# Performance work log

Hardware: AMD Instinct MI355X
Metric: run time of the kernel (lower is better)

The kernel has to match this reference:

```python
import jax, jax.numpy as jnp
import numpy as np

# Geometry: 256x256 image, 16x16 superpixel grid (cell=16), K=256, C=20 features, B=4.
B, H, W, C, KG = 4, 256, 256, 20, 16
K = KG * KG
CELL = H // KG
BIG_DIST = 1e4  # additive distance for non-neighbor superpixels


def setup_inputs() -> dict:
    key = jax.random.key(0)
    kf, = jax.random.split(key, 1)
    # initial hard pixel->superpixel grid assignment (get_spixel_init)
    gy = jnp.arange(H) // CELL
    gx = jnp.arange(W) // CELL
    spixel_init = (gy[:, None] * KG + gx[None, :]).reshape(-1).astype(jnp.int32)  # [N]
    # 9-neighborhood validity mask (compute_neighbor_spix_idx)
    ky = jnp.arange(K) // KG
    kx = jnp.arange(K) % KG
    pgy = spixel_init // KG
    pgx = spixel_init % KG
    valid = ((jnp.abs(pgy[:, None] - ky[None, :]) <= 1)
             & (jnp.abs(pgx[:, None] - kx[None, :]) <= 1)).astype(jnp.float32)  # [N, K]
    adjust = (1.0 - valid) * BIG_DIST  # [N, K]
    features = jax.random.normal(kf, (B, H * W, C), dtype=jnp.float32)  # CNN output, flattened
    return {
        "features": features,
        "valid_spixel": valid,
        "adjust_dist": adjust,
        "spixel_init": spixel_init,
        "iter_EM": 10,
    }


def _e_step(mean, features, valid_spixel, adjust_dist):
    # squared distances via ||f||^2 - 2 f.m + ||m||^2 (bmm form)
    feat_sq = jnp.sum(features * features, axis=-1)        # [B, N]
    mean_sq = jnp.sum(mean * mean, axis=-1)                # [B, K]
    dot = jnp.einsum('bnc,bkc->bnk', features, mean)       # [B, N, K]
    dist_sq = feat_sq[:, :, None] - 2.0 * dot + mean_sq[:, None, :]
    dist_sq = dist_sq * valid_spixel[None] + adjust_dist[None]
    # std = 1/sqrt(2) => 2*std^2 = 1, so softmax argument is -dist_sq
    return jax.nn.softmax(-dist_sq, axis=2)                # [B, N, K]


def _m_step(features, posteriors):
    # L1-normalize posteriors over the pixel axis (dim=1), then weighted mean
    col = jnp.maximum(jnp.sum(posteriors, axis=1, keepdims=True), 1e-12)
    post_norm = posteriors / col
    return jnp.einsum('bnk,bnc->bkc', post_norm, features)  # [B, K, C]


def reference(features, valid_spixel, adjust_dist, spixel_init, iter_EM):
    # compute_init_spixel_feat: mean of features within each initial superpixel (detached in torch)
    n = features.shape[1]
    sums = jax.vmap(lambda f: jax.ops.segment_sum(f, spixel_init, num_segments=K))(features)  # [B, K, C]
    counts = jax.ops.segment_sum(jnp.ones((n,), features.dtype), spixel_init, num_segments=K)  # [K]
    mean = jax.lax.stop_gradient(sums / jnp.maximum(counts, 1.0)[None, :, None])
    for _ in range(int(iter_EM) - 1):
        posteriors = _e_step(mean, features, valid_spixel, adjust_dist)
        mean = _m_step(features, posteriors)
    return _e_step(mean, features, valid_spixel, adjust_dist)
```

## Files before the change

kernel.cpp:

```cpp
#include <hip/hip_runtime.h>


#define NBATCH 4
#define WIMG   256
#define NC     20
#define NCS    21
#define NKG    16
#define NK     256
#define NPIX   65536
#define CELLSZ 16
#define LDST   260
#define NBLK   (NBATCH * NK)
#define CPAD   64
#define NCTRL  (NBATCH * NK)

typedef float nfloat4 __attribute__((ext_vector_type(4)));

__device__ __forceinline__ float dot4f(const float4 a, const float4 b) {
    return fmaf(a.x, b.x, fmaf(a.y, b.y, fmaf(a.z, b.z, a.w * b.w)));
}

__device__ __forceinline__ float sys_load(const float* p) {
    return __hip_atomic_load(p, __ATOMIC_RELAXED, __HIP_MEMORY_SCOPE_SYSTEM);
}
__device__ __forceinline__ void sys_store(float* p, float v) {
    __hip_atomic_store(p, v, __ATOMIC_RELAXED, __HIP_MEMORY_SCOPE_SYSTEM);
}
__device__ __forceinline__ unsigned sys_loadu(const unsigned* p) {
    return __hip_atomic_load(p, __ATOMIC_RELAXED, __HIP_MEMORY_SCOPE_SYSTEM);
}

__device__ __forceinline__ void wait_slots(const unsigned* ctr, unsigned gen,
                                           int b, int cy, int cx, int t) {
    if (t < 9) {
        int ky = cy + t / 3 - 1, kx = cx + (t % 3) - 1;
        if (ky >= 0 && ky < NKG && kx >= 0 && kx < NKG) {
            int ry = 1 + (ky > 0) + (ky < NKG - 1);
            int rx = 1 + (kx > 0) + (kx < NKG - 1);
            unsigned tgt = gen * (unsigned)(ry * rx);
            const unsigned* p = ctr + (size_t)(b * NK + ky * NKG + kx) * CPAD;
            unsigned long long t0 = __builtin_amdgcn_s_memrealtime();
            while (sys_loadu(p) < tgt) {
                __builtin_amdgcn_s_sleep(2);
                if (__builtin_amdgcn_s_memrealtime() - t0 > 10000000ull) break;
            }
        }
    }
    __syncthreads();
}

__device__ __forceinline__ void signal_slots(unsigned* ctr, int b, int cy, int cx, int t) {
    if (t < 9) {
        int ky = cy + t / 3 - 1, kx = cx + (t % 3) - 1;
        if (ky >= 0 && ky < NKG && kx >= 0 && kx < NKG)
            __hip_atomic_fetch_add(ctr + (size_t)(b * NK + ky * NKG + kx) * CPAD, 1u,
                                   __ATOMIC_RELAXED, __HIP_MEMORY_SCOPE_SYSTEM);
    }
}

__device__ __forceinline__ void load_feat(const float* __restrict__ feat, int b, int n, float f[NC]) {
    const float4* fp = (const float4*)(feat + ((size_t)b * NPIX + n) * NC);
    #pragma unroll
    for (int i = 0; i < 5; ++i) {
        float4 v = fp[i];
        f[4 * i + 0] = v.x; f[4 * i + 1] = v.y; f[4 * i + 2] = v.z; f[4 * i + 3] = v.w;
    }
}

__device__ __forceinline__ void stage_neigh(const float* __restrict__ Sprev, int b, int cy, int cx,
                                            int t, float (*sM)[24], float (*rqs)[2]) {
    if (t < 189) {
        int j = t / 21, c = t - 21 * j;
        int ky = cy + j / 3 - 1, kx = cx + (j % 3) - 1;
        float v = 0.0f;
        if (ky >= 0 && ky < NKG && kx >= 0 && kx < NKG)
            v = sys_load(&Sprev[((size_t)(b * NK + ky * NKG + kx)) * NCS + c]);
        sM[j][c] = v;
    }
    __syncthreads();
    if (t < 9) {
        int ky = cy + t / 3 - 1, kx = cx + (t % 3) - 1;
        bool ok = (ky >= 0 && ky < NKG && kx >= 0 && kx < NKG);
        float ssq = 0.f;
        #pragma unroll
        for (int cq = 0; cq < 5; ++cq) {
            float4 sv = *((const float4*)&sM[t][4 * cq]);
            ssq += dot4f(sv, sv);
        }
        float r = 1.0f / fmaxf(sM[t][NC], 1e-12f);
        rqs[t][0] = ok ? 2.0f * r : 0.0f;
        rqs[t][1] = ok ? -(r * r) * ssq : -1e30f;
    }
    __syncthreads();
}

__device__ __forceinline__ void e_step_lds(const float f[NC], const float (*sM)[24],
                                           const float (*rqs)[2], float p[9]) {
    float a[9];
    float amax = -1e30f;
    #pragma unroll
    for (int j = 0; j < 9; ++j) {
        float dots = 0.f;
        #pragma unroll
        for (int cq = 0; cq < 5; ++cq) {
            float4 sv = *((const float4*)&sM[j][4 * cq]);
            dots = fmaf(f[4 * cq + 0], sv.x,
                   fmaf(f[4 * cq + 1], sv.y,
                   fmaf(f[4 * cq + 2], sv.z,
                   fmaf(f[4 * cq + 3], sv.w, dots))));
        }
        float2 rv = *((const float2*)rqs[j]);
        a[j] = fmaf(rv.x, dots, rv.y);
        amax = fmaxf(amax, a[j]);
    }
    float esum = 0.f;
    #pragma unroll
    for (int j = 0; j < 9; ++j) {
        float e = (a[j] > -1e29f) ? __expf(a[j] - amax) : 0.0f;
        p[j] = e;
        esum += e;
    }
    float inv = 1.0f / esum;
    #pragma unroll
    for (int j = 0; j < 9; ++j) p[j] *= inv;
}

__global__ void k_zero_ctr(unsigned* ctr) {
    int i = blockIdx.x * 256 + threadIdx.x;
    if (i < NCTRL) ctr[(size_t)i * CPAD] = 0u;
}

__global__ __launch_bounds__(256, 4) void k_fused(const float* __restrict__ feat,
                                                  float* __restrict__ b0,
                                                  float* __restrict__ b1,
                                                  float* __restrict__ b2,
                                                  unsigned* __restrict__ ctr,
                                                  float* __restrict__ out) {
    __shared__ float fT[NCS * LDST];
    __shared__ float pT[9 * LDST];
    __shared__ float part[21 * 8 * 9];
    __shared__ float sM[9][24];
    __shared__ float rqs[9][2];

    int blk = blockIdx.x;
    int b = blk >> 8, k0 = blk & 255;
    int cy = k0 >> 4, cx = k0 & 15;
    int t = threadIdx.x;
    int ly = t >> 4, lx = t & 15;
    int n = (cy * CELLSZ + ly) * WIMG + cx * CELLSZ + lx;

    float f[NC];
    load_feat(feat, b, n, f);
    #pragma unroll
    for (int c = 0; c < NC; ++c) fT[c * LDST + t] = f[c];
    fT[NC * LDST + t] = 1.0f;
    __syncthreads();

    if (t < NCS) {
        float s;
        if (t == NC) {
            s = 256.0f;
        } else {
            s = 0.f;
            const float4* row = (const float4*)&fT[t * LDST];
            #pragma unroll 4
            for (int i = 0; i < 64; ++i) { float4 v = row[i]; s += v.x + v.y + v.z + v.w; }
        }
        size_t off = ((size_t)(b * NK + k0)) * NCS + t;
        sys_store(&b0[off], s);
        sys_store(&b1[off], 0.0f);
    }
    __syncthreads();
    signal_slots(ctr, b, cy, cx, t);
    unsigned gen = 1;

    float* Sprev = b0; float* Snext = b1; float* Szero = b2;

    for (int it = 0; it < 9; ++it) {
        wait_slots(ctr, gen, b, cy, cx, t);
        stage_neigh(Sprev, b, cy, cx, t, sM, rqs);

        float p[9];
        e_step_lds(f, sM, rqs, p);
        #pragma unroll
        for (int j = 0; j < 9; ++j) pT[j * LDST + t] = p[j];
        __syncthreads();

        if (t < 168) {
            int tile = t >> 3, kid = t & 7;
            int j0 = (tile / 7) * 3, c0 = (tile % 7) * 3;
            float acc[3][3] = {};
            #pragma unroll
            for (int ch = 0; ch < 8; ++ch) {
                int nb = kid * 32 + (((ch + kid) & 7) << 2);
                float4 pv[3], fv[3];
                #pragma unroll
                for (int jj = 0; jj < 3; ++jj) pv[jj] = *(const float4*)&pT[(j0 + jj) * LDST + nb];
                #pragma unroll
                for (int cc = 0; cc < 3; ++cc) fv[cc] = *(const float4*)&fT[(c0 + cc) * LDST + nb];
                #pragma unroll
                for (int jj = 0; jj < 3; ++jj)
                    #pragma unroll
                    for (int cc = 0; cc < 3; ++cc)
                        acc[jj][cc] += dot4f(pv[jj], fv[cc]);
            }
            #pragma unroll
            for (int jj = 0; jj < 3; ++jj)
                #pragma unroll
                for (int cc = 0; cc < 3; ++cc)
                    part[tile * 72 + kid * 9 + jj * 3 + cc] = acc[jj][cc];
        }
        __syncthreads();
        if (t < 189) {
            int j = t / 21, c = t - 21 * j;
            int tile = (j / 3) * 7 + (c / 3);
            int elem = (j % 3) * 3 + (c % 3);
            float s = 0.f;
            #pragma unroll
            for (int kid = 0; kid < 8; ++kid) s += part[tile * 72 + kid * 9 + elem];
            int ky = cy + (j / 3) - 1, kx = cx + (j % 3) - 1;
            if (ky >= 0 && ky < NKG && kx >= 0 && kx < NKG)
                atomicAdd(&Snext[((size_t)(b * NK + ky * NKG + kx)) * NCS + c], s);
        }
        if (t < NCS) sys_store(&Szero[((size_t)(b * NK + k0)) * NCS + t], 0.0f);
        __syncthreads();
        signal_slots(ctr, b, cy, cx, t);
        ++gen;
        float* tmp = Sprev; Sprev = Snext; Snext = Szero; Szero = tmp;
    }

    wait_slots(ctr, gen, b, cy, cx, t);
    stage_neigh(Sprev, b, cy, cx, t, sM, rqs);
    {
        float p[9];
        e_step_lds(f, sM, rqs, p);
        #pragma unroll
        for (int j = 0; j < 9; ++j) pT[j * LDST + t] = p[j];
    }
    __syncthreads();

    int wv = t >> 6, ln = t & 63;
    int j4[4];
    #pragma unroll
    for (int q = 0; q < 4; ++q) {
        int k = 4 * ln + q;
        int ky = k >> 4, kx = k & 15;
        int dy = ky - cy, dx = kx - cx;
        j4[q] = (dy >= -1 && dy <= 1 && dx >= -1 && dx <= 1) ? (dy + 1) * 3 + (dx + 1) : -1;
    }
    for (int i = 0; i < 64; ++i) {
        int pix = wv * 64 + i;
        int py = pix >> 4, px = pix & 15;
        int np = (cy * CELLSZ + py) * WIMG + cx * CELLSZ + px;
        nfloat4 o;
        o.x = (j4[0] >= 0) ? pT[j4[0] * LDST + pix] : 0.0f;
        o.y = (j4[1] >= 0) ? pT[j4[1] * LDST + pix] : 0.0f;
        o.z = (j4[2] >= 0) ? pT[j4[2] * LDST + pix] : 0.0f;
        o.w = (j4[3] >= 0) ? pT[j4[3] * LDST + pix] : 0.0f;
        size_t rowoff = ((size_t)(b * NPIX + np)) * (size_t)NK;
        __builtin_nontemporal_store(o, (nfloat4*)(out + rowoff + 4 * ln));
    }
}


__device__ __forceinline__ void e_step_global(const float* f, int b, int cy, int cx,
                                              const float* __restrict__ Sprev, float p[9]) {
    float a[9];
    float amax = -1e30f;
    #pragma unroll
    for (int dy = -1; dy <= 1; ++dy) {
        #pragma unroll
        for (int dx = -1; dx <= 1; ++dx) {
            int j = (dy + 1) * 3 + (dx + 1);
            int ky = cy + dy, kx = cx + dx;
            if (ky >= 0 && ky < NKG && kx >= 0 && kx < NKG) {
                const float* sp = Sprev + ((size_t)(b * NK + ky * NKG + kx)) * NCS;
                float dots = 0.f, ssq = 0.f;
                #pragma unroll
                for (int c = 0; c < NC; ++c) {
                    float sv = sp[c];
                    dots = fmaf(f[c], sv, dots);
                    ssq  = fmaf(sv, sv, ssq);
                }
                float col = fmaxf(sp[NC], 1e-12f);
                float r = 1.0f / col;
                a[j] = 2.0f * r * dots - (r * r) * ssq;
                amax = fmaxf(amax, a[j]);
            } else {
                a[j] = -1e30f;
            }
        }
    }
    float esum = 0.f;
    #pragma unroll
    for (int j = 0; j < 9; ++j) {
        float e = (a[j] > -1e29f) ? __expf(a[j] - amax) : 0.0f;
        p[j] = e;
        esum += e;
    }
    float inv = 1.0f / esum;
    #pragma unroll
    for (int j = 0; j < 9; ++j) p[j] *= inv;
}

__global__ __launch_bounds__(256, 4) void k_init(const float* __restrict__ feat,
                                                 float* __restrict__ S0,
                                                 float* __restrict__ S1) {
    __shared__ float fT[NC * LDST];
    int blk = blockIdx.x;
    int b = blk >> 8, k0 = blk & 255;
    int cy = k0 >> 4, cx = k0 & 15;
    int t = threadIdx.x;
    int ly = t >> 4, lx = t & 15;
    int n = (cy * CELLSZ + ly) * WIMG + cx * CELLSZ + lx;
    float f[NC];
    load_feat(feat, b, n, f);
    #pragma unroll
    for (int c = 0; c < NC; ++c) fT[c * LDST + t] = f[c];
    __syncthreads();
    if (t < NCS) {
        float s;
        if (t == NC) {
            s = 256.0f;
        } else {
            s = 0.f;
            const float4* row = (const float4*)&fT[t * LDST];
            #pragma unroll 4
            for (int i = 0; i < 64; ++i) { float4 v = row[i]; s += v.x + v.y + v.z + v.w; }
        }
        size_t off = ((size_t)(b * NK + k0)) * NCS + t;
        S0[off] = s;
        S1[off] = 0.0f;
    }
}

__global__ __launch_bounds__(256, 4) void k_em(const float* __restrict__ feat,
                                               const float* __restrict__ Sprev,
                                               float* __restrict__ Snext,
                                               float* __restrict__ Szero) {
    __shared__ float fT[NCS * LDST];
    __shared__ float pT[9 * LDST];
    __shared__ float part[21 * 8 * 9];
    int blk = blockIdx.x;
    int b = blk >> 8, k0 = blk & 255;
    int cy = k0 >> 4, cx = k0 & 15;
    int t = threadIdx.x;
    int ly = t >> 4, lx = t & 15;
    int n = (cy * CELLSZ + ly) * WIMG + cx * CELLSZ + lx;
    float f[NC];
    load_feat(feat, b, n, f);
    #pragma unroll
    for (int c = 0; c < NC; ++c) fT[c * LDST + t] = f[c];
    fT[NC * LDST + t] = 1.0f;
    float p[9];
    e_step_global(f, b, cy, cx, Sprev, p);
    #pragma unroll
    for (int j = 0; j < 9; ++j) pT[j * LDST + t] = p[j];
    __syncthreads();

    if (t < 168) {
        int tile = t >> 3, kid = t & 7;
        int j0 = (tile / 7) * 3, c0 = (tile % 7) * 3;
        float acc[3][3] = {};
        #pragma unroll
        for (int ch = 0; ch < 8; ++ch) {
            int nb = kid * 32 + (((ch + kid) & 7) << 2);
            float4 pv[3], fv[3];
            #pragma unroll
            for (int jj = 0; jj < 3; ++jj) pv[jj] = *(const float4*)&pT[(j0 + jj) * LDST + nb];
            #pragma unroll
            for (int cc = 0; cc < 3; ++cc) fv[cc] = *(const float4*)&fT[(c0 + cc) * LDST + nb];
            #pragma unroll
            for (int jj = 0; jj < 3; ++jj)
                #pragma unroll
                for (int cc = 0; cc < 3; ++cc)
                    acc[jj][cc] += dot4f(pv[jj], fv[cc]);
        }
        #pragma unroll
        for (int jj = 0; jj < 3; ++jj)
            #pragma unroll
            for (int cc = 0; cc < 3; ++cc)
                part[tile * 72 + kid * 9 + jj * 3 + cc] = acc[jj][cc];
    }
    __syncthreads();
    if (t < 189) {
        int j = t / 21, c = t % 21;
        int tile = (j / 3) * 7 + (c / 3);
        int elem = (j % 3) * 3 + (c % 3);
        float s = 0.f;
        #pragma unroll
        for (int kid = 0; kid < 8; ++kid) s += part[tile * 72 + kid * 9 + elem];
        int ky = cy + (j / 3) - 1, kx = cx + (j % 3) - 1;
        if (ky >= 0 && ky < NKG && kx >= 0 && kx < NKG)
            atomicAdd(&Snext[((size_t)(b * NK + ky * NKG + kx)) * NCS + c], s);
    }
    if (t < NCS) Szero[((size_t)(b * NK + k0)) * NCS + t] = 0.0f;
}

__global__ __launch_bounds__(256, 4) void k_final(const float* __restrict__ feat,
                                                  const float* __restrict__ Sprev,
                                                  float* __restrict__ out) {
    __shared__ float pT[9 * LDST];
    int blk = blockIdx.x;
    int b = blk >> 8, k0 = blk & 255;
    int cy = k0 >> 4, cx = k0 & 15;
    int t = threadIdx.x;
    int ly = t >> 4, lx = t & 15;
    int n = (cy * CELLSZ + ly) * WIMG + cx * CELLSZ + lx;
    float f[NC];
    load_feat(feat, b, n, f);
    float p[9];
    e_step_global(f, b, cy, cx, Sprev, p);
    #pragma unroll
    for (int j = 0; j < 9; ++j) pT[j * LDST + t] = p[j];
    __syncthreads();

    int wv = t >> 6, ln = t & 63;
    int j4[4];
    #pragma unroll
    for (int q = 0; q < 4; ++q) {
        int k = 4 * ln + q;
        int ky = k >> 4, kx = k & 15;
        int dy = ky - cy, dx = kx - cx;
        j4[q] = (dy >= -1 && dy <= 1 && dx >= -1 && dx <= 1) ? (dy + 1) * 3 + (dx + 1) : -1;
    }
    for (int i = 0; i < 64; ++i) {
        int pix = wv * 64 + i;
        int py = pix >> 4, px = pix & 15;
        int np = (cy * CELLSZ + py) * WIMG + cx * CELLSZ + px;
        float4 o;
        o.x = (j4[0] >= 0) ? pT[j4[0] * LDST + pix] : 0.0f;
        o.y = (j4[1] >= 0) ? pT[j4[1] * LDST + pix] : 0.0f;
        o.z = (j4[2] >= 0) ? pT[j4[2] * LDST + pix] : 0.0f;
        o.w = (j4[3] >= 0) ? pT[j4[3] * LDST + pix] : 0.0f;
        size_t rowoff = ((size_t)(b * NPIX + np)) * (size_t)NK;
        *(float4*)(out + rowoff + 4 * ln) = o;
    }
}

extern "C" void kernel_launch(void* const* d_in, const int* in_sizes, int n_in,
                              void* d_out, int out_size, void* d_ws, size_t ws_size,
                              hipStream_t stream) {
    (void)in_sizes; (void)n_in; (void)out_size; (void)ws_size;
    const float* feat = (const float*)d_in[0];
    float* out = (float*)d_out;
    const size_t SB = (size_t)NBATCH * NK * NCS;
    float* b0 = (float*)d_ws;
    float* b1 = b0 + SB;
    float* b2 = b1 + SB;
    unsigned* ctr = (unsigned*)((char*)d_ws + (256 << 10));

    dim3 grid(NBLK), block(256);
    k_zero_ctr<<<4, 256, 0, stream>>>(ctr);

    void* args[] = { (void*)&feat, (void*)&b0, (void*)&b1, (void*)&b2, (void*)&ctr, (void*)&out };
    hipError_t err = hipLaunchCooperativeKernel((const void*)k_fused, grid, block,
                                                (void**)args, 0u, stream);
    if (err != hipSuccess) {
        float* bufs[3] = { b0, b1, b2 };
        k_init<<<grid, block, 0, stream>>>(feat, bufs[0], bufs[1]);
        for (int i = 1; i <= 9; ++i) {
            k_em<<<grid, block, 0, stream>>>(feat, bufs[(i - 1) % 3], bufs[i % 3], bufs[(i + 1) % 3]);
        }
        k_final<<<grid, block, 0, stream>>>(feat, bufs[0], out);
    }
}
```

Baseline: 610.3 us.

## Replace atomicAdd scatter with per-block partial stores and owner-side gather

```diff
diff --git a/kernel.cpp b/kernel.cpp
--- a/kernel.cpp
+++ b/kernel.cpp
@@ -12,7 +12,8 @@
 #define LDST   260
 #define NBLK   (NBATCH * NK)
 #define CPAD   64
-#define NCTRL  (NBATCH * NK)
+#define SB     ((size_t)NBATCH * NK * NCS)
+#define PBLK   (9 * NCS)
 
 typedef float nfloat4 __attribute__((ext_vector_type(4)));
 
@@ -29,16 +30,16 @@
 __device__ __forceinline__ unsigned sys_loadu(const unsigned* p) {
     return __hip_atomic_load(p, __ATOMIC_RELAXED, __HIP_MEMORY_SCOPE_SYSTEM);
 }
-
-__device__ __forceinline__ void wait_slots(const unsigned* ctr, unsigned gen,
-                                           int b, int cy, int cx, int t) {
+__device__ __forceinline__ void sys_storeu(unsigned* p, unsigned v) {
+    __hip_atomic_store(p, v, __ATOMIC_RELAXED, __HIP_MEMORY_SCOPE_SYSTEM);
+}
+
+__device__ __forceinline__ void wait_rc(const unsigned* rc, unsigned tgt,
+                                        int b, int cy, int cx, int t) {
     if (t < 9) {
         int ky = cy + t / 3 - 1, kx = cx + (t % 3) - 1;
         if (ky >= 0 && ky < NKG && kx >= 0 && kx < NKG) {
-            int ry = 1 + (ky > 0) + (ky < NKG - 1);
-            int rx = 1 + (kx > 0) + (kx < NKG - 1);
-            unsigned tgt = gen * (unsigned)(ry * rx);
-            const unsigned* p = ctr + (size_t)(b * NK + ky * NKG + kx) * CPAD;
+            const unsigned* p = rc + (size_t)(b * NK + ky * NKG + kx) * CPAD;
             unsigned long long t0 = __builtin_amdgcn_s_memrealtime();
             while (sys_loadu(p) < tgt) {
                 __builtin_amdgcn_s_sleep(2);
@@ -47,15 +48,6 @@
         }
     }
     __syncthreads();
-}
-
-__device__ __forceinline__ void signal_slots(unsigned* ctr, int b, int cy, int cx, int t) {
-    if (t < 9) {
-        int ky = cy + t / 3 - 1, kx = cx + (t % 3) - 1;
-        if (ky >= 0 && ky < NKG && kx >= 0 && kx < NKG)
-            __hip_atomic_fetch_add(ctr + (size_t)(b * NK + ky * NKG + kx) * CPAD, 1u,
-                                   __ATOMIC_RELAXED, __HIP_MEMORY_SCOPE_SYSTEM);
-    }
 }
 
 __device__ __forceinline__ void load_feat(const float* __restrict__ feat, int b, int n, float f[NC]) {
@@ -125,16 +117,17 @@
     for (int j = 0; j < 9; ++j) p[j] *= inv;
 }
 
+#define NZLINES (2 * NBLK)
 __global__ void k_zero_ctr(unsigned* ctr) {
     int i = blockIdx.x * 256 + threadIdx.x;
-    if (i < NCTRL) ctr[(size_t)i * CPAD] = 0u;
+    if (i < NZLINES) ctr[(size_t)i * CPAD] = 0u;
 }
 
 __global__ __launch_bounds__(256, 4) void k_fused(const float* __restrict__ feat,
-                                                  float* __restrict__ b0,
-                                                  float* __restrict__ b1,
-                                                  float* __restrict__ b2,
-                                                  unsigned* __restrict__ ctr,
+                                                  float* __restrict__ Sbuf,
+                                                  float* __restrict__ Pp,
+                                                  unsigned* __restrict__ rc,
+                                                  unsigned* __restrict__ cc,
                                                   float* __restrict__ out) {
     __shared__ float fT[NCS * LDST];
     __shared__ float pT[9 * LDST];
@@ -148,6 +141,8 @@
     int t = threadIdx.x;
     int ly = t >> 4, lx = t & 15;
     int n = (cy * CELLSZ + ly) * WIMG + cx * CELLSZ + lx;
+    int slot = b * NK + k0;
+    int cnt_k = (1 + (cy > 0) + (cy < NKG - 1)) * (1 + (cx > 0) + (cx < NKG - 1));
 
     float f[NC];
     load_feat(feat, b, n, f);
@@ -166,18 +161,17 @@
             #pragma unroll 4
             for (int i = 0; i < 64; ++i) { float4 v = row[i]; s += v.x + v.y + v.z + v.w; }
         }
-        size_t off = ((size_t)(b * NK + k0)) * NCS + t;
-        sys_store(&b0[off], s);
-        sys_store(&b1[off], 0.0f);
-    }
-    __syncthreads();
-    signal_slots(ctr, b, cy, cx, t);
-    unsigned gen = 1;
-
-    float* Sprev = b0; float* Snext = b1; float* Szero = b2;
-
-    for (int it = 0; it < 9; ++it) {
-        wait_slots(ctr, gen, b, cy, cx, t);
+        sys_store(&Sbuf[(size_t)slot * NCS + t], s);
+    }
+    __syncthreads();
+    if (t == 0) sys_storeu(rc + (size_t)slot * CPAD, 1u);
+
+    for (unsigned g = 1; g <= 9; ++g) {
+        const float* Sprev = Sbuf + (size_t)((g - 1) & 1) * SB;
+        float*       Snew  = Sbuf + (size_t)(g & 1) * SB;
+        float*       Pcur  = Pp + (size_t)(g & 1) * NBLK * PBLK;
+
+        wait_rc(rc, g, b, cy, cx, t);
         stage_neigh(Sprev, b, cy, cx, t, sM, rqs);
 
         float p[9];
@@ -197,20 +191,21 @@
                 #pragma unroll
                 for (int jj = 0; jj < 3; ++jj) pv[jj] = *(const float4*)&pT[(j0 + jj) * LDST + nb];
                 #pragma unroll
-                for (int cc = 0; cc < 3; ++cc) fv[cc] = *(const float4*)&fT[(c0 + cc) * LDST + nb];
+                for (int cc2 = 0; cc2 < 3; ++cc2) fv[cc2] = *(const float4*)&fT[(c0 + cc2) * LDST + nb];
                 #pragma unroll
                 for (int jj = 0; jj < 3; ++jj)
                     #pragma unroll
-                    for (int cc = 0; cc < 3; ++cc)
-                        acc[jj][cc] += dot4f(pv[jj], fv[cc]);
+                    for (int cc2 = 0; cc2 < 3; ++cc2)
+                        acc[jj][cc2] += dot4f(pv[jj], fv[cc2]);
             }
             #pragma unroll
             for (int jj = 0; jj < 3; ++jj)
                 #pragma unroll
-                for (int cc = 0; cc < 3; ++cc)
-                    part[tile * 72 + kid * 9 + jj * 3 + cc] = acc[jj][cc];
-        }
-        __syncthreads();
+                for (int cc2 = 0; cc2 < 3; ++cc2)
+                    part[tile * 72 + kid * 9 + jj * 3 + cc2] = acc[jj][cc2];
+        }
+        __syncthreads();
+
         if (t < 189) {
             int j = t / 21, c = t - 21 * j;
             int tile = (j / 3) * 7 + (c / 3);
@@ -218,19 +213,51 @@
             float s = 0.f;
             #pragma unroll
             for (int kid = 0; kid < 8; ++kid) s += part[tile * 72 + kid * 9 + elem];
-            int ky = cy + (j / 3) - 1, kx = cx + (j % 3) - 1;
+            sys_store(&Pcur[(size_t)blk * PBLK + t], s);
+        }
+        __syncthreads();
+        if (t < 9) {
+            int ky = cy + t / 3 - 1, kx = cx + (t % 3) - 1;
             if (ky >= 0 && ky < NKG && kx >= 0 && kx < NKG)
-                atomicAdd(&Snext[((size_t)(b * NK + ky * NKG + kx)) * NCS + c], s);
-        }
-        if (t < NCS) sys_store(&Szero[((size_t)(b * NK + k0)) * NCS + t], 0.0f);
-        __syncthreads();
-        signal_slots(ctr, b, cy, cx, t);
-        ++gen;
-        float* tmp = Sprev; Sprev = Snext; Snext = Szero; Szero = tmp;
-    }
-
-    wait_slots(ctr, gen, b, cy, cx, t);
-    stage_neigh(Sprev, b, cy, cx, t, sM, rqs);
+                __hip_atomic_fetch_add(cc + (size_t)(b * NK + ky * NKG + kx) * CPAD, 1u,
+                                       __ATOMIC_RELAXED, __HIP_MEMORY_SCOPE_SYSTEM);
+        }
+
+        if (t == 0) {
+            const unsigned* p = cc + (size_t)slot * CPAD;
+            unsigned tgt = g * (unsigned)cnt_k;
+            unsigned long long t0 = __builtin_amdgcn_s_memrealtime();
+            while (sys_loadu(p) < tgt) {
+                __builtin_amdgcn_s_sleep(2);
+                if (__builtin_amdgcn_s_memrealtime() - t0 > 10000000ull) break;
+            }
+        }
+        __syncthreads();
+
+        if (t < 189) {
+            int j = t / 21, c = t - 21 * j;
+            int my = cy + j / 3 - 1, mx = cx + (j % 3) - 1;
+            float v = 0.0f;
+            if (my >= 0 && my < NKG && mx >= 0 && mx < NKG) {
+                int mblk = b * NK + my * NKG + mx;
+                v = sys_load(&Pcur[(size_t)mblk * PBLK + (8 - j) * NCS + c]);
+            }
+            part[j * NCS + c] = v;
+        }
+        __syncthreads();
+
+        if (t < NCS) {
+            float s = 0.f;
+            #pragma unroll
+            for (int j = 0; j < 9; ++j) s += part[j * NCS + t];
+            sys_store(&Snew[(size_t)slot * NCS + t], s);
+        }
+        __syncthreads();
+        if (t == 0) sys_storeu(rc + (size_t)slot * CPAD, g + 1);
+    }
+
+    wait_rc(rc, 10u, b, cy, cx, t);
+    stage_neigh(Sbuf + SB, b, cy, cx, t, sM, rqs);
     {
         float p[9];
         e_step_lds(f, sM, rqs, p);
@@ -369,18 +396,18 @@
             #pragma unroll
             for (int jj = 0; jj < 3; ++jj) pv[jj] = *(const float4*)&pT[(j0 + jj) * LDST + nb];
             #pragma unroll
-            for (int cc = 0; cc < 3; ++cc) fv[cc] = *(const float4*)&fT[(c0 + cc) * LDST + nb];
+            for (int cc2 = 0; cc2 < 3; ++cc2) fv[cc2] = *(const float4*)&fT[(c0 + cc2) * LDST + nb];
             #pragma unroll
             for (int jj = 0; jj < 3; ++jj)
                 #pragma unroll
-                for (int cc = 0; cc < 3; ++cc)
-                    acc[jj][cc] += dot4f(pv[jj], fv[cc]);
+                for (int cc2 = 0; cc2 < 3; ++cc2)
+                    acc[jj][cc2] += dot4f(pv[jj], fv[cc2]);
         }
         #pragma unroll
         for (int jj = 0; jj < 3; ++jj)
             #pragma unroll
-            for (int cc = 0; cc < 3; ++cc)
-                part[tile * 72 + kid * 9 + jj * 3 + cc] = acc[jj][cc];
+            for (int cc2 = 0; cc2 < 3; ++cc2)
+                part[tile * 72 + kid * 9 + jj * 3 + cc2] = acc[jj][cc2];
     }
     __syncthreads();
     if (t < 189) {
@@ -444,21 +471,23 @@
     (void)in_sizes; (void)n_in; (void)out_size; (void)ws_size;
     const float* feat = (const float*)d_in[0];
     float* out = (float*)d_out;
-    const size_t SB = (size_t)NBATCH * NK * NCS;
-    float* b0 = (float*)d_ws;
-    float* b1 = b0 + SB;
-    float* b2 = b1 + SB;
-    unsigned* ctr = (unsigned*)((char*)d_ws + (256 << 10));
+    float* Sbuf = (float*)d_ws;
+    unsigned* rc = (unsigned*)((char*)d_ws + (256 << 10));
+    unsigned* cc = (unsigned*)((char*)d_ws + (256 << 10) + (size_t)NBLK * CPAD * 4);
+    float* Pp = (float*)((char*)d_ws + (1 << 20));
 
     dim3 grid(NBLK), block(256);
-    k_zero_ctr<<<4, 256, 0, stream>>>(ctr);
-
-    void* args[] = { (void*)&feat, (void*)&b0, (void*)&b1, (void*)&b2, (void*)&ctr, (void*)&out };
+    k_zero_ctr<<<8, 256, 0, stream>>>(rc);
+
+    void* args[] = { (void*)&feat, (void*)&Sbuf, (void*)&Pp, (void*)&rc, (void*)&cc, (void*)&out };
     hipError_t err = hipLaunchCooperativeKernel((const void*)k_fused, grid, block,
                                                 (void**)args, 0u, stream);
     if (err != hipSuccess) {
+        float* b0 = Pp;
+        float* b1 = b0 + SB;
+        float* b2 = b1 + SB;
+        k_init<<<grid, block, 0, stream>>>(feat, b0, b1);
         float* bufs[3] = { b0, b1, b2 };
-        k_init<<<grid, block, 0, stream>>>(feat, bufs[0], bufs[1]);
         for (int i = 1; i <= 9; ++i) {
             k_em<<<grid, block, 0, stream>>>(feat, bufs[(i - 1) % 3], bufs[i % 3], bufs[(i + 1) % 3]);
         }
```

Measured after the change: 632.1 us. 3.6% more time.
